# Performance work log

Hardware: AMD Instinct MI355X
Metric: run time of the kernel (lower is better)

## Reference

```python
import jax, jax.numpy as jnp
import numpy as np


def _rotation_matrix(orientation):
    # orientation = [roll, pitch, yaw]; R = RX @ RY @ RZ, matching the torch module.
    roll, pitch, yaw = orientation[0], orientation[1], orientation[2]
    cr, sr = jnp.cos(roll), jnp.sin(roll)
    cp, sp = jnp.cos(pitch), jnp.sin(pitch)
    cy, sy = jnp.cos(yaw), jnp.sin(yaw)
    one = jnp.ones((), dtype=orientation.dtype)
    zero = jnp.zeros((), dtype=orientation.dtype)
    RX = jnp.stack([
        jnp.stack([one, zero, zero]),
        jnp.stack([zero, cr, -sr]),
        jnp.stack([zero, sr, cr]),
    ])
    RY = jnp.stack([
        jnp.stack([cp, zero, sp]),
        jnp.stack([zero, one, zero]),
        jnp.stack([-sp, zero, cp]),
    ])
    RZ = jnp.stack([
        jnp.stack([cy, -sy, zero]),
        jnp.stack([sy, cy, zero]),
        jnp.stack([zero, zero, one]),
    ])
    return RX @ RY @ RZ  # [3, 3]


def setup_inputs() -> dict:
    key = jax.random.key(0)
    k1, k2, k3 = jax.random.split(key, 3)
    B, N = 2048, 6890  # batch of SMPL meshes, 6890 vertices each
    joints = jax.random.normal(k1, (B, N, 3), dtype=jnp.float32)
    # orientation initialized like xavier_uniform then clamped to [-pi/4, pi/4]
    orientation = jnp.clip(
        jax.random.normal(k2, (3,), dtype=jnp.float32) * 0.5,
        -np.pi * 0.25, np.pi * 0.25,
    )
    translation = jax.random.normal(k3, (3,), dtype=jnp.float32) * 0.1
    return {"joints": joints, "orientation": orientation, "translation": translation}


def reference(joints, orientation, translation):
    R = _rotation_matrix(orientation)  # [3, 3]
    # joints: [..., 3] -> rotated + translated
    return joints @ R + translation
```

## Files before the change

kernel.cpp:

```cpp
#include <hip/hip_runtime.h>


using f4 = __attribute__((ext_vector_type(4))) float;

__global__ __launch_bounds__(256) void Transform_38723425141290_kernel(
    const float* __restrict__ joints,
    const float* __restrict__ orient,
    const float* __restrict__ trans,
    float* __restrict__ out,
    long long n_groups,
    long long n_points)
{
    const float roll = orient[0], pitch = orient[1], yaw = orient[2];
    const float sr = __sinf(roll),  cr = __cosf(roll);
    const float sp = __sinf(pitch), cp = __cosf(pitch);
    const float sy = __sinf(yaw),   cy = __cosf(yaw);

    const float R00 = cp * cy;
    const float R01 = -cp * sy;
    const float R02 = sp;
    const float R10 = sr * sp * cy + cr * sy;
    const float R11 = cr * cy - sr * sp * sy;
    const float R12 = -sr * cp;
    const float R20 = sr * sy - cr * sp * cy;
    const float R21 = cr * sp * sy + sr * cy;
    const float R22 = cr * cp;

    const float tx = trans[0], ty = trans[1], tz = trans[2];

    const long long g = (long long)blockIdx.x * blockDim.x + threadIdx.x;

    if (g < n_groups) {
        const f4* jp = reinterpret_cast<const f4*>(joints) + g * 6;
        f4 a = jp[0], b = jp[1], c = jp[2], d = jp[3], e = jp[4], f = jp[5];

        f4 o0, o1, o2, o3, o4, o5;
        #define ROT(x, y, z, ox, oy, oz)              \
            ox = x * R00 + y * R10 + z * R20 + tx;    \
            oy = x * R01 + y * R11 + z * R21 + ty;    \
            oz = x * R02 + y * R12 + z * R22 + tz;

        ROT(a.x, a.y, a.z, o0.x, o0.y, o0.z)
        ROT(a.w, b.x, b.y, o0.w, o1.x, o1.y)
        ROT(b.z, b.w, c.x, o1.z, o1.w, o2.x)
        ROT(c.y, c.z, c.w, o2.y, o2.z, o2.w)
        ROT(d.x, d.y, d.z, o3.x, o3.y, o3.z)
        ROT(d.w, e.x, e.y, o3.w, o4.x, o4.y)
        ROT(e.z, e.w, f.x, o4.z, o4.w, o5.x)
        ROT(f.y, f.z, f.w, o5.y, o5.z, o5.w)
        #undef ROT

        f4* op = reinterpret_cast<f4*>(out) + g * 6;
        op[0] = o0;
        op[1] = o1;
        op[2] = o2;
        op[3] = o3;
        op[4] = o4;
        op[5] = o5;
    }

    const long long tail_base = n_groups * 8;
    if (g < (n_points - tail_base)) {
        const long long i = tail_base + g;
        const float x = joints[i * 3 + 0];
        const float y = joints[i * 3 + 1];
        const float z = joints[i * 3 + 2];
        out[i * 3 + 0] = x * R00 + y * R10 + z * R20 + tx;
        out[i * 3 + 1] = x * R01 + y * R11 + z * R21 + ty;
        out[i * 3 + 2] = x * R02 + y * R12 + z * R22 + tz;
    }
}

extern "C" void kernel_launch(void* const* d_in, const int* in_sizes, int n_in,
                              void* d_out, int out_size, void* d_ws, size_t ws_size,
                              hipStream_t stream) {
    const float* joints = (const float*)d_in[0];
    const float* orient = (const float*)d_in[1];
    const float* trans  = (const float*)d_in[2];
    float* out = (float*)d_out;

    const long long n_floats = (long long)in_sizes[0];
    const long long n_points = n_floats / 3;
    const long long n_groups = n_points / 8;

    const int block = 256;
    long long work = n_groups > 0 ? n_groups : 1;
    const long long grid = (work + block - 1) / block;

    Transform_38723425141290_kernel<<<dim3((unsigned)grid), dim3(block), 0, stream>>>(
        joints, orient, trans, out, n_groups, n_points);
}
```

Baseline: 297.6 us.

## Stage joints through swizzled LDS for fully coalesced float4 loads and stores

Each block now loads its contiguous chunk of joints with lane-contiguous float4 accesses into shared memory using an XOR swizzle, syncs, and has each thread read its six float4s (eight points) from LDS. Results are written back to LDS and then stored to global memory in the same coalesced pattern. This targets the strided 96-byte-per-thread global access of the old kernel. It adds two barriers and LDS traffic per block, and partial blocks fall back to a scalar loop.

```diff
diff --git a/kernel.cpp b/kernel.cpp
--- a/kernel.cpp
+++ b/kernel.cpp
@@ -3,14 +3,22 @@
 
 using f4 = __attribute__((ext_vector_type(4))) float;
 
-__global__ __launch_bounds__(256) void Transform_38723425141290_kernel(
+#define BLOCK 256
+#define F4_PER_THREAD 6
+#define F4_PER_BLOCK (BLOCK * F4_PER_THREAD)
+#define PTS_PER_BLOCK ((F4_PER_BLOCK * 4) / 3)
+
+__device__ __forceinline__ int swz(int i) { return i ^ ((i >> 3) & 7); }
+
+__global__ __launch_bounds__(BLOCK) void Transform_38723425141290_kernel(
     const float* __restrict__ joints,
     const float* __restrict__ orient,
     const float* __restrict__ trans,
     float* __restrict__ out,
-    long long n_groups,
     long long n_points)
 {
+    __shared__ f4 lds[F4_PER_BLOCK];
+
     const float roll = orient[0], pitch = orient[1], yaw = orient[2];
     const float sr = __sinf(roll),  cr = __cosf(roll);
     const float sp = __sinf(pitch), cp = __cosf(pitch);
@@ -28,11 +36,24 @@
 
     const float tx = trans[0], ty = trans[1], tz = trans[2];
 
-    const long long g = (long long)blockIdx.x * blockDim.x + threadIdx.x;
+    const int tid = threadIdx.x;
+    const long long blk = blockIdx.x;
 
-    if (g < n_groups) {
-        const f4* jp = reinterpret_cast<const f4*>(joints) + g * 6;
-        f4 a = jp[0], b = jp[1], c = jp[2], d = jp[3], e = jp[4], f = jp[5];
+    if ((blk + 1) * (long long)PTS_PER_BLOCK <= n_points) {
+        const long long f4_base = blk * (long long)F4_PER_BLOCK;
+        const f4* jp = reinterpret_cast<const f4*>(joints) + f4_base;
+
+        #pragma unroll
+        for (int k = 0; k < F4_PER_THREAD; ++k)
+            lds[swz(k * BLOCK + tid)] = jp[k * BLOCK + tid];
+        __syncthreads();
+
+        f4 a = lds[swz(tid * 6 + 0)];
+        f4 b = lds[swz(tid * 6 + 1)];
+        f4 c = lds[swz(tid * 6 + 2)];
+        f4 d = lds[swz(tid * 6 + 3)];
+        f4 e = lds[swz(tid * 6 + 4)];
+        f4 f = lds[swz(tid * 6 + 5)];
 
         f4 o0, o1, o2, o3, o4, o5;
         #define ROT(x, y, z, ox, oy, oz)              \
@@ -50,24 +71,28 @@
         ROT(f.y, f.z, f.w, o5.y, o5.z, o5.w)
         #undef ROT
 
-        f4* op = reinterpret_cast<f4*>(out) + g * 6;
-        op[0] = o0;
-        op[1] = o1;
-        op[2] = o2;
-        op[3] = o3;
-        op[4] = o4;
-        op[5] = o5;
-    }
+        lds[swz(tid * 6 + 0)] = o0;
+        lds[swz(tid * 6 + 1)] = o1;
+        lds[swz(tid * 6 + 2)] = o2;
+        lds[swz(tid * 6 + 3)] = o3;
+        lds[swz(tid * 6 + 4)] = o4;
+        lds[swz(tid * 6 + 5)] = o5;
+        __syncthreads();
 
-    const long long tail_base = n_groups * 8;
-    if (g < (n_points - tail_base)) {
-        const long long i = tail_base + g;
-        const float x = joints[i * 3 + 0];
-        const float y = joints[i * 3 + 1];
-        const float z = joints[i * 3 + 2];
-        out[i * 3 + 0] = x * R00 + y * R10 + z * R20 + tx;
-        out[i * 3 + 1] = x * R01 + y * R11 + z * R21 + ty;
-        out[i * 3 + 2] = x * R02 + y * R12 + z * R22 + tz;
+        f4* op = reinterpret_cast<f4*>(out) + f4_base;
+        #pragma unroll
+        for (int k = 0; k < F4_PER_THREAD; ++k)
+            op[k * BLOCK + tid] = lds[swz(k * BLOCK + tid)];
+    } else {
+        for (long long p = blk * (long long)PTS_PER_BLOCK + tid; p < n_points;
+             p += BLOCK) {
+            const float x = joints[p * 3 + 0];
+            const float y = joints[p * 3 + 1];
+            const float z = joints[p * 3 + 2];
+            out[p * 3 + 0] = x * R00 + y * R10 + z * R20 + tx;
+            out[p * 3 + 1] = x * R01 + y * R11 + z * R21 + ty;
+            out[p * 3 + 2] = x * R02 + y * R12 + z * R22 + tz;
+        }
     }
 }
 
@@ -81,12 +106,10 @@
 
     const long long n_floats = (long long)in_sizes[0];
     const long long n_points = n_floats / 3;
-    const long long n_groups = n_points / 8;
 
-    const int block = 256;
-    long long work = n_groups > 0 ? n_groups : 1;
-    const long long grid = (work + block - 1) / block;
+    const long long grid =
+        (n_points + PTS_PER_BLOCK - 1) / PTS_PER_BLOCK;
 
-    Transform_38723425141290_kernel<<<dim3((unsigned)grid), dim3(block), 0, stream>>>(
-        joints, orient, trans, out, n_groups, n_points);
+    Transform_38723425141290_kernel<<<dim3((unsigned)grid), dim3(BLOCK), 0, stream>>>(
+        joints, orient, trans, out, n_points);
 }
```

After: 289.3 us. 2.8% less time.

## Use grid-stride loop with software-prefetched 4-point groups and capped grid

Applied to the files above, without the earlier changes.

Switches from one thread per 8-point group over a full grid to a grid-stride loop over 4-point groups (3 float4 loads each). The grid is capped at 2048 blocks, and the next iteration's loads are issued before the current group is computed and stored, to overlap memory latency. This lowers per-thread register use and spreads the work across persistent threads. The trade-off is a longer per-thread loop with fewer waves in flight, which may expose latency on a bandwidth-bound streaming kernel.

```diff
diff --git a/kernel.cpp b/kernel.cpp
--- a/kernel.cpp
+++ b/kernel.cpp
@@ -3,7 +3,10 @@
 
 using f4 = __attribute__((ext_vector_type(4))) float;
 
-__global__ __launch_bounds__(256) void Transform_38723425141290_kernel(
+#define BLOCK 256
+#define MAX_BLOCKS 2048
+
+__global__ __launch_bounds__(BLOCK) void Transform_38723425141290_kernel(
     const float* __restrict__ joints,
     const float* __restrict__ orient,
     const float* __restrict__ trans,
@@ -28,40 +31,53 @@
 
     const float tx = trans[0], ty = trans[1], tz = trans[2];
 
-    const long long g = (long long)blockIdx.x * blockDim.x + threadIdx.x;
+    const long long stride = (long long)gridDim.x * blockDim.x;
+    long long g = (long long)blockIdx.x * blockDim.x + threadIdx.x;
+
+    const f4* __restrict__ jp = reinterpret_cast<const f4*>(joints);
+    f4* __restrict__ op = reinterpret_cast<f4*>(out);
 
     if (g < n_groups) {
-        const f4* jp = reinterpret_cast<const f4*>(joints) + g * 6;
-        f4 a = jp[0], b = jp[1], c = jp[2], d = jp[3], e = jp[4], f = jp[5];
+        f4 a = jp[g * 3 + 0];
+        f4 b = jp[g * 3 + 1];
+        f4 c = jp[g * 3 + 2];
 
-        f4 o0, o1, o2, o3, o4, o5;
-        #define ROT(x, y, z, ox, oy, oz)              \
-            ox = x * R00 + y * R10 + z * R20 + tx;    \
-            oy = x * R01 + y * R11 + z * R21 + ty;    \
-            oz = x * R02 + y * R12 + z * R22 + tz;
+        for (;;) {
+            const long long gn = g + stride;
+            const bool more = (gn < n_groups);
+            f4 a2, b2, c2;
+            if (more) {
+                a2 = jp[gn * 3 + 0];
+                b2 = jp[gn * 3 + 1];
+                c2 = jp[gn * 3 + 2];
+            }
 
-        ROT(a.x, a.y, a.z, o0.x, o0.y, o0.z)
-        ROT(a.w, b.x, b.y, o0.w, o1.x, o1.y)
-        ROT(b.z, b.w, c.x, o1.z, o1.w, o2.x)
-        ROT(c.y, c.z, c.w, o2.y, o2.z, o2.w)
-        ROT(d.x, d.y, d.z, o3.x, o3.y, o3.z)
-        ROT(d.w, e.x, e.y, o3.w, o4.x, o4.y)
-        ROT(e.z, e.w, f.x, o4.z, o4.w, o5.x)
-        ROT(f.y, f.z, f.w, o5.y, o5.z, o5.w)
-        #undef ROT
+            f4 o0, o1, o2;
+            #define ROT(x, y, z, ox, oy, oz)              \
+                ox = x * R00 + y * R10 + z * R20 + tx;    \
+                oy = x * R01 + y * R11 + z * R21 + ty;    \
+                oz = x * R02 + y * R12 + z * R22 + tz;
 
-        f4* op = reinterpret_cast<f4*>(out) + g * 6;
-        op[0] = o0;
-        op[1] = o1;
-        op[2] = o2;
-        op[3] = o3;
-        op[4] = o4;
-        op[5] = o5;
+            ROT(a.x, a.y, a.z, o0.x, o0.y, o0.z)
+            ROT(a.w, b.x, b.y, o0.w, o1.x, o1.y)
+            ROT(b.z, b.w, c.x, o1.z, o1.w, o2.x)
+            ROT(c.y, c.z, c.w, o2.y, o2.z, o2.w)
+            #undef ROT
+
+            op[g * 3 + 0] = o0;
+            op[g * 3 + 1] = o1;
+            op[g * 3 + 2] = o2;
+
+            if (!more) break;
+            g = gn;
+            a = a2; b = b2; c = c2;
+        }
     }
 
-    const long long tail_base = n_groups * 8;
-    if (g < (n_points - tail_base)) {
-        const long long i = tail_base + g;
+    const long long tail_base = n_groups * 4;
+    const long long t0 = (long long)blockIdx.x * blockDim.x + threadIdx.x;
+    if (t0 < (n_points - tail_base)) {
+        const long long i = tail_base + t0;
         const float x = joints[i * 3 + 0];
         const float y = joints[i * 3 + 1];
         const float z = joints[i * 3 + 2];
@@ -81,12 +97,12 @@
 
     const long long n_floats = (long long)in_sizes[0];
     const long long n_points = n_floats / 3;
-    const long long n_groups = n_points / 8;
+    const long long n_groups = n_points / 4;
 
-    const int block = 256;
-    long long work = n_groups > 0 ? n_groups : 1;
-    const long long grid = (work + block - 1) / block;
+    long long blocks = (n_groups + BLOCK - 1) / BLOCK;
+    if (blocks > MAX_BLOCKS) blocks = MAX_BLOCKS;
+    if (blocks < 1) blocks = 1;
 
-    Transform_38723425141290_kernel<<<dim3((unsigned)grid), dim3(block), 0, stream>>>(
+    Transform_38723425141290_kernel<<<dim3((unsigned)blocks), dim3(BLOCK), 0, stream>>>(
         joints, orient, trans, out, n_groups, n_points);
 }
```

Measured after the change: 295.0 us. Within noise of the previous version (-0.9%).
